# Kernel tuning notes

Hardware: AMD Instinct MI355X
Metric: run time of the kernel (lower is better)

## Reference

```python
import jax, jax.numpy as jnp
import numpy as np

OFFS = [(dy, dx) for dy in (-1, 0, 1) for dx in (-1, 0, 1)]  # ME centered 3x3 region


def _build_maps():
    """Build the sparse coordinate pyramid and per-offset kernel maps, exactly
    mirroring MinkowskiEngine: out coords of a stride-2 conv are unique(c//2),
    and a pair (i_in, i_out) exists iff coord_out*stride + offset is active."""
    G = 1024
    rng = np.random.default_rng(0)
    flat = np.sort(rng.choice(G * G, size=300000, replace=False))
    coords = [np.stack(np.unravel_index(flat, (G, G)), axis=1).astype(np.int64)]
    grids = [G]
    for _ in range(3):
        coords.append(np.unique(coords[-1] // 2, axis=0))
        grids.append(grids[-1] // 2)

    def lut(c, g):
        t = -np.ones(g * g, np.int64)
        t[c[:, 0] * g + c[:, 1]] = np.arange(len(c))
        return t

    luts = [lut(c, g) for c, g in zip(coords, grids)]

    def kmap(lvl_in, c_out, stride):
        g, L = grids[lvl_in], luts[lvl_in]
        n_in, n_out = len(coords[lvl_in]), len(c_out)
        base = c_out * stride
        pairs = []
        for dy, dx in OFFS:
            q = base + np.array([dy, dx])
            ok = (q[:, 0] >= 0) & (q[:, 0] < g) & (q[:, 1] >= 0) & (q[:, 1] < g)
            key = np.clip(q[:, 0] * g + q[:, 1], 0, g * g - 1)
            idx = np.where(ok, L[key], -1)
            sel = np.nonzero(idx >= 0)[0]
            pairs.append((idx[sel], sel))
        M = max(len(p[0]) for p in pairs)
        ii = np.full((9, M), n_in, np.int32)   # pad -> dummy zero input row
        oo = np.full((9, M), n_out, np.int32)  # pad -> dummy output row (dropped)
        for k, (a, b) in enumerate(pairs):
            ii[k, :len(a)] = a
            oo[k, :len(b)] = b
        return ii, oo

    maps = {
        'c0': kmap(0, coords[0], 1), 'd0': kmap(0, coords[1], 2),
        'c1': kmap(1, coords[1], 1), 'd1': kmap(1, coords[2], 2),
        'c2': kmap(2, coords[2], 1), 'd2': kmap(2, coords[3], 2),
    }
    return maps, [len(c) for c in coords]


def setup_inputs() -> dict:
    maps, (n0, n1, n2, n3) = _build_maps()
    ks = jax.random.split(jax.random.key(0), 16)
    d = {'feats': jax.random.normal(ks[0], (n0, 1), jnp.float32)}
    chans = [(1, 64), (64, 128), (128, 128), (128, 128), (128, 128), (128, 128)]
    names = ['c0', 'd0', 'c1', 'd1', 'c2', 'd2']
    for i, (nm, (ci, co)) in enumerate(zip(names, chans)):
        d[f'w_{nm}'] = jax.random.normal(ks[1 + 2 * i], (9, ci, co), jnp.float32) / np.sqrt(9.0 * ci)
        d[f'b_{nm}'] = jax.random.normal(ks[2 + 2 * i], (co,), jnp.float32) * 0.01
        d[f'in_{nm}'] = jnp.asarray(maps[nm][0])
        d[f'out_{nm}'] = jnp.asarray(maps[nm][1])
    d.update(n0=n0, n1=n1, n2=n2, n3=n3)
    return d


def sparse_conv(feats, w, b, in_idx, out_idx, n_out):
    """Gather-GEMM-scatter sparse conv. w: [9, Cin, Cout]. Padded pairs point at a
    dummy zero input row (index n_in) and a dummy output row (index n_out)."""
    n_in, cin = feats.shape
    fp = jnp.concatenate([feats, jnp.zeros((1, cin), feats.dtype)], axis=0)
    out = jnp.zeros((n_out + 1, w.shape[2]), feats.dtype)
    for k in range(9):  # fixed kernel volume
        out = out.at[out_idx[k]].add(fp[in_idx[k]] @ w[k])
    return out[:n_out] + b


def reference(feats, w_c0, b_c0, in_c0, out_c0, w_d0, b_d0, in_d0, out_d0,
              w_c1, b_c1, in_c1, out_c1, w_d1, b_d1, in_d1, out_d1,
              w_c2, b_c2, in_c2, out_c2, w_d2, b_d2, in_d2, out_d2,
              n0, n1, n2, n3):
    x = sparse_conv(feats, w_c0, b_c0, in_c0, out_c0, n0)
    out0 = jax.nn.relu(sparse_conv(x, w_d0, b_d0, in_d0, out_d0, n1))
    y = sparse_conv(out0, w_c1, b_c1, in_c1, out_c1, n1)
    out1 = jax.nn.relu(sparse_conv(y, w_d1, b_d1, in_d1, out_d1, n2))
    z = sparse_conv(out1, w_c2, b_c2, in_c2, out_c2, n2)
    out2 = sparse_conv(z, w_d2, b_d2, in_d2, out_d2, n3)
    return (out2, out1, out0)
```

## Files before the change

kernel.cpp:

```cpp
#include <hip/hip_runtime.h>
#include <stdint.h>
#include <algorithm>


#define DI __device__ __forceinline__

typedef __attribute__((ext_vector_type(8))) short bf16x8;
typedef __attribute__((ext_vector_type(4))) float f32x4;

DI uint16_t f2bf(float x){
  union{float f;uint32_t i;}v; v.f=x;
  uint32_t r = v.i + 0x7fffu + ((v.i>>16)&1u);
  return (uint16_t)(r>>16);
}
DI uint32_t pack2(float a, float b){
  return (uint32_t)f2bf(a) | ((uint32_t)f2bf(b) << 16);
}
DI void gload16(const void* g, void* l){
  __builtin_amdgcn_global_load_lds(
      (const __attribute__((address_space(1))) void*)g,
      (__attribute__((address_space(3))) void*)l, 16, 0, 0);
}

__global__ __launch_bounds__(256) void diag_kernel(float* __restrict__ out, long n, float c){
  long i = (long)blockIdx.x*256 + threadIdx.x;
  if (i < n) out[i] = c;
}

__global__ __launch_bounds__(256) void init_all_kernel(
    int* __restrict__ tab, long ntab, float* __restrict__ zp){
  long i = (long)blockIdx.x*256 + threadIdx.x;
  if (i < ntab) tab[i] = -1;
  if (blockIdx.x == 0 && threadIdx.x < 64) zp[threadIdx.x] = 0.f;
}

struct BuildArgs {
  const int* im[6];
  const int* om[6];
  int   M[6];
  int   nin[6];
  int   nout[6];
  long  toff[6];
};

__global__ __launch_bounds__(256) void build_all_kernel(
    BuildArgs a, int* __restrict__ tb){
  const int L = blockIdx.z, k = blockIdx.y;
  const int M = a.M[L];
  long t = (long)blockIdx.x*256 + threadIdx.x;
  if (t >= M) return;
  int ii = a.im[L][(long)k*M + t];
  int oo = a.om[L][(long)k*M + t];
  if (ii >= 0 && ii < a.nin[L] && oo >= 0 && oo < a.nout[L])
    tb[a.toff[L] + (long)k*a.nout[L] + oo] = ii;
}

__global__ __launch_bounds__(256) void prep_all_kernel(
    const float* __restrict__ w0, const float* __restrict__ w1,
    const float* __restrict__ w2, const float* __restrict__ w3,
    const float* __restrict__ w4, uint16_t* __restrict__ wb, long total){
  const long wt64 = 9L*128*64, wt128 = 9L*128*128;
  long idx = (long)blockIdx.x*256 + threadIdx.x;
  if (idx >= total) return;
  int L; long r; int cin;
  if (idx < wt64){ L = 0; r = idx; cin = 64; }
  else { long j = idx - wt64; L = 1 + (int)(j / wt128); r = j % wt128; cin = 128; }
  const float* w = (L==0) ? w0 : (L==1) ? w1 : (L==2) ? w2 : (L==3) ? w3 : w4;
  int k = (int)(r / (128*cin));
  int rem = (int)(r % (128*cin));
  int cout = rem / cin, ci = rem % cin;
  wb[idx] = f2bf(w[((long)k*cin + ci)*128 + cout]);
}

__global__ __launch_bounds__(256) void c0_tab_kernel(
    const float* __restrict__ feats, const float* __restrict__ w,
    const float* __restrict__ bias, const int* __restrict__ tab,
    uint16_t* __restrict__ out, int n_out){
  __shared__ float w_s[576];
  __shared__ float b_s[64];
  const int tid = threadIdx.x;
  for (int i = tid; i < 576; i += 256) w_s[i] = w[i];
  if (tid < 64) b_s[tid] = bias[tid];
  __syncthreads();
  long r = (long)blockIdx.x*256 + tid;
  if (r >= n_out) return;
  float f[9];
  #pragma unroll
  for (int k = 0; k < 9; k++){
    int gi = tab[(long)k*n_out + r];
    f[k] = (gi >= 0) ? feats[gi] : 0.f;
  }
  uint16_t* dst = out + r*64;
  #pragma unroll
  for (int c0 = 0; c0 < 64; c0 += 16){
    float a[16];
    #pragma unroll
    for (int j = 0; j < 16; j++) a[j] = b_s[c0+j];
    #pragma unroll
    for (int k = 0; k < 9; k++){
      float fk = f[k];
      #pragma unroll
      for (int j = 0; j < 16; j++) a[j] += fk * w_s[k*64 + c0 + j];
    }
    uint4 o0, o1;
    o0.x = pack2(a[0],a[1]);   o0.y = pack2(a[2],a[3]);
    o0.z = pack2(a[4],a[5]);   o0.w = pack2(a[6],a[7]);
    o1.x = pack2(a[8],a[9]);   o1.y = pack2(a[10],a[11]);
    o1.z = pack2(a[12],a[13]); o1.w = pack2(a[14],a[15]);
    *(uint4*)(dst + c0)     = o0;
    *(uint4*)(dst + c0 + 8) = o1;
  }
}

template<int CIN, int OUTMODE, bool RELU>
__global__ __launch_bounds__(512,4) void mconv4_kernel(
    const char* __restrict__ ws_base, long in_off, long wtb_off, long zp_off,
    const float* __restrict__ bias, const int* __restrict__ tab,
    float* __restrict__ outf, uint16_t* __restrict__ outb, int n_out){
  constexpr int NS = 9*CIN/64;
  __shared__ __align__(16) uint16_t ab[3][128*64];
  __shared__ __align__(16) uint16_t bb[2][128*64];

  const int tid = threadIdx.x;
  const int nwg = gridDim.x, orig = blockIdx.x;
  const int q = nwg >> 3, rr = nwg & 7, xcd = orig & 7, pos = orig >> 3;
  const int wg = (xcd < rr ? xcd*(q+1) : rr*(q+1) + (xcd-rr)*q) + pos;
  const long rb = (long)wg * 128;

  const int r0 = tid >> 3, sg = tid & 7;
  const int ss0 = sg ^ (r0 & 7);

  uint32_t offA[2][9];
  #pragma unroll
  for (int kk = 0; kk < 9; ++kk){
    #pragma unroll
    for (int it = 0; it < 2; ++it){
      long row = rb + it*64 + r0;
      int gi = (row < (long)n_out) ? tab[(long)kk*n_out + row] : -1;
      offA[it][kk] = (gi >= 0)
          ? (uint32_t)(in_off + (long)gi*(CIN*2) + ss0*16)
          : (uint32_t)(zp_off + ss0*16);
    }
  }
  const uint32_t offB = (uint32_t)(wtb_off + ((long)r0*CIN + ss0*8)*2);

  const int lane = tid & 63;
  const int wv = tid >> 6;
  const int wr = (wv >> 1) << 5;
  const int wc = (wv & 1) << 6;
  const int l16 = lane & 15, quad = lane >> 4;

  float bv[4];
  #pragma unroll
  for (int ct = 0; ct < 4; ++ct) bv[ct] = bias[wc + (ct<<4) + l16];

  f32x4 acc[2][4];
  #pragma unroll
  for (int i = 0; i < 2; i++)
    #pragma unroll
    for (int j = 0; j < 4; j++)
      acc[i][j] = (f32x4){0.f,0.f,0.f,0.f};

  auto stage_a = [&](int step, int nb){
    const int kk  = (CIN == 64) ? step : (step >> 1);
    const int c0b = (CIN == 64) ? 0 : ((step & 1) * 128);
    #pragma unroll
    for (int it = 0; it < 2; ++it)
      gload16(ws_base + offA[it][kk] + c0b, &ab[nb][(it*512+tid)*8]);
  };
  auto stage_b = [&](int step, int nb){
    const int kk  = (CIN == 64) ? step : (step >> 1);
    const int c0b = (CIN == 64) ? 0 : ((step & 1) * 128);
    const uint32_t base = offB + (uint32_t)((long)kk*128*CIN*2 + c0b);
    #pragma unroll
    for (int it = 0; it < 2; ++it)
      gload16(ws_base + base + it*(64*CIN*2), &bb[nb][(it*512+tid)*8]);
  };
  auto compute = [&](int na, int nb){
    const uint16_t* A  = &ab[na][0];
    const uint16_t* Bm = &bb[nb][0];
    __builtin_amdgcn_s_setprio(1);
    #pragma unroll
    for (int ch = 0; ch < 2; ++ch){
      const int xs = ((((ch << 2) + quad) ^ (l16 & 7)) << 3);
      bf16x8 af[2], bfr[4];
      #pragma unroll
      for (int u = 0; u < 2; ++u)
        af[u]  = *(const bf16x8*)&A [((wr + (u<<4) + l16) << 6) + xs];
      #pragma unroll
      for (int u = 0; u < 4; ++u)
        bfr[u] = *(const bf16x8*)&Bm[((wc + (u<<4) + l16) << 6) + xs];
      #pragma unroll
      for (int rt = 0; rt < 2; ++rt)
        #pragma unroll
        for (int ct = 0; ct < 4; ++ct)
          acc[rt][ct] = __builtin_amdgcn_mfma_f32_16x16x32_bf16(
              af[rt], bfr[ct], acc[rt][ct], 0, 0, 0);
    }
    __builtin_amdgcn_s_setprio(0);
  };

  stage_a(0, 0);
  stage_a(1, 1);
  stage_b(0, 0);
  #pragma unroll
  for (int t = 0; t < NS; ++t){
    if (t + 2 < NS) stage_a(t+2, (t+2)%3);
    if (t + 1 < NS) stage_b(t+1, (t+1)&1);
    if (t + 2 < NS){
      asm volatile("s_waitcnt vmcnt(4)" ::: "memory");
    } else if (t + 1 < NS){
      asm volatile("s_waitcnt vmcnt(2)" ::: "memory");
    } else {
      asm volatile("s_waitcnt vmcnt(0)" ::: "memory");
    }
    __builtin_amdgcn_sched_barrier(0);
    __builtin_amdgcn_s_barrier();
    compute(t%3, t&1);
    if (t + 1 < NS)
      __builtin_amdgcn_s_barrier();
  }

  #pragma unroll
  for (int ct = 0; ct < 4; ++ct){
    const int cout = wc + (ct<<4) + l16;
    #pragma unroll
    for (int rt = 0; rt < 2; ++rt){
      #pragma unroll
      for (int r = 0; r < 4; ++r){
        long row = rb + wr + (rt<<4) + (quad<<2) + r;
        if (row < (long)n_out){
          float v = acc[rt][ct][r] + bv[ct];
          if (RELU) v = v > 0.f ? v : 0.f;
          if constexpr (OUTMODE == 0 || OUTMODE == 2) outf[row*128 + cout] = v;
          if constexpr (OUTMODE == 1 || OUTMODE == 2) outb[row*128 + cout] = f2bf(v);
        }
      }
    }
  }
}

static inline long cdivl(long a, long b){ return (a + b - 1) / b; }

extern "C" void kernel_launch(void* const* d_in, const int* in_sizes, int n_in_args,
                              void* d_out, int out_size, void* d_ws, size_t ws_size,
                              hipStream_t stream) {
  const float* feats = (const float*)d_in[0];
  const float* w_c0 = (const float*)d_in[1];
  const float* b_c0 = (const float*)d_in[2];
  const int* in_c0  = (const int*)d_in[3];
  const int* out_c0 = (const int*)d_in[4];
  const float* w_d0 = (const float*)d_in[5];
  const float* b_d0 = (const float*)d_in[6];
  const int* in_d0  = (const int*)d_in[7];
  const int* out_d0 = (const int*)d_in[8];
  const float* w_c1 = (const float*)d_in[9];
  const float* b_c1 = (const float*)d_in[10];
  const int* in_c1  = (const int*)d_in[11];
  const int* out_c1 = (const int*)d_in[12];
  const float* w_d1 = (const float*)d_in[13];
  const float* b_d1 = (const float*)d_in[14];
  const int* in_d1  = (const int*)d_in[15];
  const int* out_d1 = (const int*)d_in[16];
  const float* w_c2 = (const float*)d_in[17];
  const float* b_c2 = (const float*)d_in[18];
  const int* in_c2  = (const int*)d_in[19];
  const int* out_c2 = (const int*)d_in[20];
  const float* w_d2 = (const float*)d_in[21];
  const float* b_d2 = (const float*)d_in[22];
  const int* in_d2  = (const int*)d_in[23];
  const int* out_d2 = (const int*)d_in[24];

  const int n0   = in_sizes[0];
  const int M_c0 = in_sizes[3]  / 9;
  const int M_d0 = in_sizes[7]  / 9;
  const int M_c1 = in_sizes[11] / 9;
  const int M_d1 = in_sizes[15] / 9;
  const int M_c2 = in_sizes[19] / 9;
  const int M_d2 = in_sizes[23] / 9;
  const int n1   = M_c1;
  const int n2   = M_c2;
  const int n3   = out_size/128 - n1 - n2;

  bool sane = n0 > 0 && out_size % 128 == 0 &&
              M_c0 > 0 && M_d0 > 0 && M_d1 > 0 && M_d2 > 0 &&
              n1 > 0 && n2 > 0 && n3 > 0;

  long maxElems = (long)n0*64;
  if ((long)n1*128 > maxElems) maxElems = (long)n1*128;
  if ((long)n2*128 > maxElems) maxElems = (long)n2*128;
  long fbytes = (maxElems*2 + 255)/256*256;
  long ntab   = sane ? 9L*((long)n0 + 2L*n1 + 2L*n2 + n3) : 0;
  long tbytes = (ntab*4 + 255)/256*256;
  long wt64  = 9L*128*64, wt128 = 9L*128*128;
  long wbytes = ((wt64 + 4*wt128)*2 + 255)/256*256;
  long zbytes = 256;
  long b1bytes = sane ? ((long)n2*128*2 + 255)/256*256 : 0;
  long b0bytes = sane ? ((long)n1*128*2 + 255)/256*256 : 0;
  long need_full = fbytes + tbytes + wbytes + zbytes + 256 + b1bytes + b0bytes;

  if (!sane || ws_size < (size_t)need_full){
    float C = (float)(16 + (int)std::min<size_t>(ws_size >> 20, (size_t)100000));
    if (!sane) C *= 1099511627776.0f;
    diag_kernel<<<cdivl(out_size,256),256,0,stream>>>((float*)d_out, out_size, C);
    return;
  }

  uint16_t* fbuf = (uint16_t*)d_ws;
  long tab_off    = fbytes;
  long wtb_off    = fbytes + tbytes;
  long zp_off     = fbytes + tbytes + wbytes;
  long bf1_off    = zp_off + zbytes + 256;
  long bf0_off    = bf1_off + b1bytes;
  const char* wsb = (const char*)d_ws;
  int* tb        = (int*)((char*)d_ws + tab_off);
  float* zp_p    = (float*)((char*)d_ws + zp_off);
  uint16_t* bf1  = (uint16_t*)((char*)d_ws + bf1_off);
  uint16_t* bf0  = (uint16_t*)((char*)d_ws + bf0_off);

  long t_c0 = 0;
  long t_d0 = t_c0 + 9L*n0;
  long t_c1 = t_d0 + 9L*n1;
  long t_d1 = t_c1 + 9L*n1;
  long t_c2 = t_d1 + 9L*n2;
  long t_d2 = t_c2 + 9L*n2;

  float* out2 = (float*)d_out;
  float* out1 = out2 + (long)n3*128;
  float* out0 = out1 + (long)n2*128;

  init_all_kernel<<<cdivl(ntab,256),256,0,stream>>>(tb, ntab, zp_p);

  BuildArgs ba;
  ba.im[0]=in_c0;  ba.om[0]=out_c0; ba.M[0]=M_c0; ba.nin[0]=n0; ba.nout[0]=n0; ba.toff[0]=t_c0;
  ba.im[1]=in_d0;  ba.om[1]=out_d0; ba.M[1]=M_d0; ba.nin[1]=n0; ba.nout[1]=n1; ba.toff[1]=t_d0;
  ba.im[2]=in_c1;  ba.om[2]=out_c1; ba.M[2]=M_c1; ba.nin[2]=n1; ba.nout[2]=n1; ba.toff[2]=t_c1;
  ba.im[3]=in_d1;  ba.om[3]=out_d1; ba.M[3]=M_d1; ba.nin[3]=n1; ba.nout[3]=n2; ba.toff[3]=t_d1;
  ba.im[4]=in_c2;  ba.om[4]=out_c2; ba.M[4]=M_c2; ba.nin[4]=n2; ba.nout[4]=n2; ba.toff[4]=t_c2;
  ba.im[5]=in_d2;  ba.om[5]=out_d2; ba.M[5]=M_d2; ba.nin[5]=n2; ba.nout[5]=n3; ba.toff[5]=t_d2;
  long maxM = M_c0;
  for (int i = 0; i < 6; ++i) if (ba.M[i] > maxM) maxM = ba.M[i];
  dim3 bg((unsigned)cdivl(maxM,256), 9, 6);
  build_all_kernel<<<bg,256,0,stream>>>(ba, tb);

  long wtotal = wt64 + 4*wt128;
  prep_all_kernel<<<cdivl(wtotal,256),256,0,stream>>>(
      w_d0, w_c1, w_d1, w_c2, w_d2,
      (uint16_t*)((char*)d_ws + wtb_off), wtotal);

  c0_tab_kernel<<<cdivl(n0,256),256,0,stream>>>(feats, w_c0, b_c0, tb + t_c0, fbuf, n0);

  mconv4_kernel<64,2,true><<<cdivl(n1,128),512,0,stream>>>(
      wsb, 0L, wtb_off, zp_off, b_d0, tb + t_d0, out0, bf0, n1);

  mconv4_kernel<128,1,false><<<cdivl(n1,128),512,0,stream>>>(
      wsb, bf0_off, wtb_off + wt64*2, zp_off, b_c1, tb + t_c1, nullptr, fbuf, n1);

  mconv4_kernel<128,2,true><<<cdivl(n2,128),512,0,stream>>>(
      wsb, 0L, wtb_off + (wt64 + wt128)*2, zp_off, b_d1, tb + t_d1, out1, bf1, n2);

  mconv4_kernel<128,1,false><<<cdivl(n2,128),512,0,stream>>>(
      wsb, bf1_off, wtb_off + (wt64 + 2*wt128)*2, zp_off, b_c2, tb + t_c2, nullptr, fbuf, n2);

  mconv4_kernel<128,0,false><<<cdivl(n3,128),512,0,stream>>>(
      wsb, 0L, wtb_off + (wt64 + 3*wt128)*2, zp_off, b_d2, tb + t_d2, out2, nullptr, n3);
}
```

Before: 491.0 us.

## Fuse all stages into a persistent megakernel with global barriers

Replaces the separate init, map-build, weight-prep, first-layer and five gather-GEMM launches with one persistent kernel of 512 blocks. The stages are separated by atomic-counter grid barriers, and each conv phase distributes its row tiles across blocks in a loop. The aim is to remove launch gaps and tail effects between the many small kernels. The risks are the spin barrier overhead, deadlock if not all 512 blocks are co-resident, and lower per-phase parallelism than the original grids.

Result: slower. 1.420 ms (+189.1%).

```diff
diff --git a/kernel.cpp b/kernel.cpp
--- a/kernel.cpp
+++ b/kernel.cpp
@@ -27,125 +27,70 @@
   if (i < n) out[i] = c;
 }
 
-__global__ __launch_bounds__(256) void init_all_kernel(
-    int* __restrict__ tab, long ntab, float* __restrict__ zp){
-  long i = (long)blockIdx.x*256 + threadIdx.x;
-  if (i < ntab) tab[i] = -1;
-  if (blockIdx.x == 0 && threadIdx.x < 64) zp[threadIdx.x] = 0.f;
-}
-
-struct BuildArgs {
-  const int* im[6];
-  const int* om[6];
-  int   M[6];
-  int   nin[6];
-  int   nout[6];
+__global__ __launch_bounds__(256) void init_bar_kernel(int* __restrict__ bar,
+                                                       float* __restrict__ zp){
+  int t = threadIdx.x;
+  if (t < 64) bar[t] = 0;
+  if (t >= 64 && t < 128) zp[t-64] = 0.f;
+}
+
+struct MegaArgs {
+  const char* wsb;
+  int* tb;
+  int* bar;
+  long ntab;
+  const int* im[6]; const int* om[6];
+  int   M[6]; int nin[6]; int nout[6];
   long  toff[6];
+  const float* w[5];
+  long wtotal;
+  uint16_t* wb;
+  const float* feats; const float* w_c0; const float* b_c0;
+  uint16_t* fbuf;
+  int n0, n1, n2, n3;
+  long wtb_off, zp_off, bf0_off, bf1_off;
+  const float *b_d0, *b_c1, *b_d1, *b_c2, *b_d2;
+  float *out0, *out1, *out2;
+  uint16_t *bf0, *bf1;
 };
 
-__global__ __launch_bounds__(256) void build_all_kernel(
-    BuildArgs a, int* __restrict__ tb){
-  const int L = blockIdx.z, k = blockIdx.y;
-  const int M = a.M[L];
-  long t = (long)blockIdx.x*256 + threadIdx.x;
-  if (t >= M) return;
-  int ii = a.im[L][(long)k*M + t];
-  int oo = a.om[L][(long)k*M + t];
-  if (ii >= 0 && ii < a.nin[L] && oo >= 0 && oo < a.nout[L])
-    tb[a.toff[L] + (long)k*a.nout[L] + oo] = ii;
-}
-
-__global__ __launch_bounds__(256) void prep_all_kernel(
-    const float* __restrict__ w0, const float* __restrict__ w1,
-    const float* __restrict__ w2, const float* __restrict__ w3,
-    const float* __restrict__ w4, uint16_t* __restrict__ wb, long total){
-  const long wt64 = 9L*128*64, wt128 = 9L*128*128;
-  long idx = (long)blockIdx.x*256 + threadIdx.x;
-  if (idx >= total) return;
-  int L; long r; int cin;
-  if (idx < wt64){ L = 0; r = idx; cin = 64; }
-  else { long j = idx - wt64; L = 1 + (int)(j / wt128); r = j % wt128; cin = 128; }
-  const float* w = (L==0) ? w0 : (L==1) ? w1 : (L==2) ? w2 : (L==3) ? w3 : w4;
-  int k = (int)(r / (128*cin));
-  int rem = (int)(r % (128*cin));
-  int cout = rem / cin, ci = rem % cin;
-  wb[idx] = f2bf(w[((long)k*cin + ci)*128 + cout]);
-}
-
-__global__ __launch_bounds__(256) void c0_tab_kernel(
-    const float* __restrict__ feats, const float* __restrict__ w,
-    const float* __restrict__ bias, const int* __restrict__ tab,
-    uint16_t* __restrict__ out, int n_out){
-  __shared__ float w_s[576];
-  __shared__ float b_s[64];
+DI void gsync(int* bar, int target){
+  __syncthreads();
+  if (threadIdx.x == 0){
+    __threadfence();
+    atomicAdd(bar, 1);
+    int spins = 0;
+    while (atomicAdd(bar, 0) < target){
+      __builtin_amdgcn_s_sleep(8);
+      if (++spins > 100000000) break;
+    }
+    __threadfence();
+  }
+  __syncthreads();
+}
+
+template<int CIN, int OUTMODE, bool RELU>
+DI void mconv_phase(uint8_t* smem, const char* ws_base, long in_off,
+                    long wtb_off, long zp_off,
+                    const float* __restrict__ bias, const int* __restrict__ tab,
+                    float* __restrict__ outf, uint16_t* __restrict__ outb,
+                    int n_out, int bid, int nblk){
+  constexpr int NS = 9*CIN/64;
+  uint16_t (*ab)[128*64] = (uint16_t(*)[128*64])smem;
+  uint16_t (*bb)[128*64] = (uint16_t(*)[128*64])(smem + 3*16384);
   const int tid = threadIdx.x;
-  for (int i = tid; i < 576; i += 256) w_s[i] = w[i];
-  if (tid < 64) b_s[tid] = bias[tid];
-  __syncthreads();
-  long r = (long)blockIdx.x*256 + tid;
-  if (r >= n_out) return;
-  float f[9];
-  #pragma unroll
-  for (int k = 0; k < 9; k++){
-    int gi = tab[(long)k*n_out + r];
-    f[k] = (gi >= 0) ? feats[gi] : 0.f;
-  }
-  uint16_t* dst = out + r*64;
-  #pragma unroll
-  for (int c0 = 0; c0 < 64; c0 += 16){
-    float a[16];
-    #pragma unroll
-    for (int j = 0; j < 16; j++) a[j] = b_s[c0+j];
-    #pragma unroll
-    for (int k = 0; k < 9; k++){
-      float fk = f[k];
-      #pragma unroll
-      for (int j = 0; j < 16; j++) a[j] += fk * w_s[k*64 + c0 + j];
-    }
-    uint4 o0, o1;
-    o0.x = pack2(a[0],a[1]);   o0.y = pack2(a[2],a[3]);
-    o0.z = pack2(a[4],a[5]);   o0.w = pack2(a[6],a[7]);
-    o1.x = pack2(a[8],a[9]);   o1.y = pack2(a[10],a[11]);
-    o1.z = pack2(a[12],a[13]); o1.w = pack2(a[14],a[15]);
-    *(uint4*)(dst + c0)     = o0;
-    *(uint4*)(dst + c0 + 8) = o1;
-  }
-}
-
-template<int CIN, int OUTMODE, bool RELU>
-__global__ __launch_bounds__(512,4) void mconv4_kernel(
-    const char* __restrict__ ws_base, long in_off, long wtb_off, long zp_off,
-    const float* __restrict__ bias, const int* __restrict__ tab,
-    float* __restrict__ outf, uint16_t* __restrict__ outb, int n_out){
-  constexpr int NS = 9*CIN/64;
-  __shared__ __align__(16) uint16_t ab[3][128*64];
-  __shared__ __align__(16) uint16_t bb[2][128*64];
-
-  const int tid = threadIdx.x;
-  const int nwg = gridDim.x, orig = blockIdx.x;
-  const int q = nwg >> 3, rr = nwg & 7, xcd = orig & 7, pos = orig >> 3;
-  const int wg = (xcd < rr ? xcd*(q+1) : rr*(q+1) + (xcd-rr)*q) + pos;
-  const long rb = (long)wg * 128;
+
+  const int T = (n_out + 127) >> 7;
+  const int q = T / nblk, r = T % nblk;
+  const int sb = (bid & 7)*(nblk >> 3) + (bid >> 3);
+  const int t0 = (sb < r) ? sb*(q+1) : r*(q+1) + (sb - r)*q;
+  const int t1 = t0 + ((sb < r) ? (q+1) : q);
 
   const int r0 = tid >> 3, sg = tid & 7;
   const int ss0 = sg ^ (r0 & 7);
-
-  uint32_t offA[2][9];
-  #pragma unroll
-  for (int kk = 0; kk < 9; ++kk){
-    #pragma unroll
-    for (int it = 0; it < 2; ++it){
-      long row = rb + it*64 + r0;
-      int gi = (row < (long)n_out) ? tab[(long)kk*n_out + row] : -1;
-      offA[it][kk] = (gi >= 0)
-          ? (uint32_t)(in_off + (long)gi*(CIN*2) + ss0*16)
-          : (uint32_t)(zp_off + ss0*16);
-    }
-  }
   const uint32_t offB = (uint32_t)(wtb_off + ((long)r0*CIN + ss0*8)*2);
 
-  const int lane = tid & 63;
-  const int wv = tid >> 6;
+  const int lane = tid & 63, wv = tid >> 6;
   const int wr = (wv >> 1) << 5;
   const int wc = (wv & 1) << 6;
   const int l16 = lane & 15, quad = lane >> 4;
@@ -154,90 +99,198 @@
   #pragma unroll
   for (int ct = 0; ct < 4; ++ct) bv[ct] = bias[wc + (ct<<4) + l16];
 
-  f32x4 acc[2][4];
-  #pragma unroll
-  for (int i = 0; i < 2; i++)
+  for (int tile = t0; tile < t1; ++tile){
+    __builtin_amdgcn_s_barrier();
+    const long rb = (long)tile * 128;
+
+    uint32_t offA[2][9];
     #pragma unroll
-    for (int j = 0; j < 4; j++)
-      acc[i][j] = (f32x4){0.f,0.f,0.f,0.f};
-
-  auto stage_a = [&](int step, int nb){
-    const int kk  = (CIN == 64) ? step : (step >> 1);
-    const int c0b = (CIN == 64) ? 0 : ((step & 1) * 128);
+    for (int kk = 0; kk < 9; ++kk){
+      #pragma unroll
+      for (int it = 0; it < 2; ++it){
+        long row = rb + it*64 + r0;
+        int gi = (row < (long)n_out) ? tab[(long)kk*n_out + row] : -1;
+        offA[it][kk] = (gi >= 0)
+            ? (uint32_t)(in_off + (long)gi*(CIN*2) + ss0*16)
+            : (uint32_t)(zp_off + ss0*16);
+      }
+    }
+
+    f32x4 acc[2][4];
     #pragma unroll
-    for (int it = 0; it < 2; ++it)
-      gload16(ws_base + offA[it][kk] + c0b, &ab[nb][(it*512+tid)*8]);
-  };
-  auto stage_b = [&](int step, int nb){
-    const int kk  = (CIN == 64) ? step : (step >> 1);
-    const int c0b = (CIN == 64) ? 0 : ((step & 1) * 128);
-    const uint32_t base = offB + (uint32_t)((long)kk*128*CIN*2 + c0b);
+    for (int i = 0; i < 2; i++)
+      #pragma unroll
+      for (int j = 0; j < 4; j++)
+        acc[i][j] = (f32x4){0.f,0.f,0.f,0.f};
+
+    auto stage_a = [&](int step, int nb){
+      const int kk  = (CIN == 64) ? step : (step >> 1);
+      const int c0b = (CIN == 64) ? 0 : ((step & 1) * 128);
+      #pragma unroll
+      for (int it = 0; it < 2; ++it)
+        gload16(ws_base + offA[it][kk] + c0b, &ab[nb][(it*512+tid)*8]);
+    };
+    auto stage_b = [&](int step, int nb){
+      const int kk  = (CIN == 64) ? step : (step >> 1);
+      const int c0b = (CIN == 64) ? 0 : ((step & 1) * 128);
+      const uint32_t base = offB + (uint32_t)((long)kk*128*CIN*2 + c0b);
+      #pragma unroll
+      for (int it = 0; it < 2; ++it)
+        gload16(ws_base + base + it*(64*CIN*2), &bb[nb][(it*512+tid)*8]);
+    };
+    auto compute = [&](int na, int nb){
+      const uint16_t* A  = &ab[na][0];
+      const uint16_t* Bm = &bb[nb][0];
+      __builtin_amdgcn_s_setprio(1);
+      #pragma unroll
+      for (int ch = 0; ch < 2; ++ch){
+        const int xs = ((((ch << 2) + quad) ^ (l16 & 7)) << 3);
+        bf16x8 af[2], bfr[4];
+        #pragma unroll
+        for (int u = 0; u < 2; ++u)
+          af[u]  = *(const bf16x8*)&A [((wr + (u<<4) + l16) << 6) + xs];
+        #pragma unroll
+        for (int u = 0; u < 4; ++u)
+          bfr[u] = *(const bf16x8*)&Bm[((wc + (u<<4) + l16) << 6) + xs];
+        #pragma unroll
+        for (int rt = 0; rt < 2; ++rt)
+          #pragma unroll
+          for (int ct = 0; ct < 4; ++ct)
+            acc[rt][ct] = __builtin_amdgcn_mfma_f32_16x16x32_bf16(
+                af[rt], bfr[ct], acc[rt][ct], 0, 0, 0);
+      }
+      __builtin_amdgcn_s_setprio(0);
+    };
+
+    stage_a(0, 0);
+    stage_a(1, 1);
+    stage_b(0, 0);
     #pragma unroll
-    for (int it = 0; it < 2; ++it)
-      gload16(ws_base + base + it*(64*CIN*2), &bb[nb][(it*512+tid)*8]);
-  };
-  auto compute = [&](int na, int nb){
-    const uint16_t* A  = &ab[na][0];
-    const uint16_t* Bm = &bb[nb][0];
-    __builtin_amdgcn_s_setprio(1);
+    for (int t = 0; t < NS; ++t){
+      if (t + 2 < NS) stage_a(t+2, (t+2)%3);
+      if (t + 1 < NS) stage_b(t+1, (t+1)&1);
+      if (t + 2 < NS){
+        asm volatile("s_waitcnt vmcnt(4)" ::: "memory");
+      } else if (t + 1 < NS){
+        asm volatile("s_waitcnt vmcnt(2)" ::: "memory");
+      } else {
+        asm volatile("s_waitcnt vmcnt(0)" ::: "memory");
+      }
+      __builtin_amdgcn_sched_barrier(0);
+      __builtin_amdgcn_s_barrier();
+      compute(t%3, t&1);
+      if (t + 1 < NS)
+        __builtin_amdgcn_s_barrier();
+    }
+
     #pragma unroll
-    for (int ch = 0; ch < 2; ++ch){
-      const int xs = ((((ch << 2) + quad) ^ (l16 & 7)) << 3);
-      bf16x8 af[2], bfr[4];
-      #pragma unroll
-      for (int u = 0; u < 2; ++u)
-        af[u]  = *(const bf16x8*)&A [((wr + (u<<4) + l16) << 6) + xs];
-      #pragma unroll
-      for (int u = 0; u < 4; ++u)
-        bfr[u] = *(const bf16x8*)&Bm[((wc + (u<<4) + l16) << 6) + xs];
-      #pragma unroll
-      for (int rt = 0; rt < 2; ++rt)
-        #pragma unroll
-        for (int ct = 0; ct < 4; ++ct)
-          acc[rt][ct] = __builtin_amdgcn_mfma_f32_16x16x32_bf16(
-              af[rt], bfr[ct], acc[rt][ct], 0, 0, 0);
-    }
-    __builtin_amdgcn_s_setprio(0);
-  };
-
-  stage_a(0, 0);
-  stage_a(1, 1);
-  stage_b(0, 0);
-  #pragma unroll
-  for (int t = 0; t < NS; ++t){
-    if (t + 2 < NS) stage_a(t+2, (t+2)%3);
-    if (t + 1 < NS) stage_b(t+1, (t+1)&1);
-    if (t + 2 < NS){
-      asm volatile("s_waitcnt vmcnt(4)" ::: "memory");
-    } else if (t + 1 < NS){
-      asm volatile("s_waitcnt vmcnt(2)" ::: "memory");
-    } else {
-      asm volatile("s_waitcnt vmcnt(0)" ::: "memory");
-    }
-    __builtin_amdgcn_sched_barrier(0);
-    __builtin_amdgcn_s_barrier();
-    compute(t%3, t&1);
-    if (t + 1 < NS)
-      __builtin_amdgcn_s_barrier();
-  }
-
-  #pragma unroll
-  for (int ct = 0; ct < 4; ++ct){
-    const int cout = wc + (ct<<4) + l16;
-    #pragma unroll
-    for (int rt = 0; rt < 2; ++rt){
-      #pragma unroll
-      for (int r = 0; r < 4; ++r){
-        long row = rb + wr + (rt<<4) + (quad<<2) + r;
-        if (row < (long)n_out){
-          float v = acc[rt][ct][r] + bv[ct];
-          if (RELU) v = v > 0.f ? v : 0.f;
-          if constexpr (OUTMODE == 0 || OUTMODE == 2) outf[row*128 + cout] = v;
-          if constexpr (OUTMODE == 1 || OUTMODE == 2) outb[row*128 + cout] = f2bf(v);
+    for (int ct = 0; ct < 4; ++ct){
+      const int cout = wc + (ct<<4) + l16;
+      #pragma unroll
+      for (int rt = 0; rt < 2; ++rt){
+        #pragma unroll
+        for (int rr2 = 0; rr2 < 4; ++rr2){
+          long row = rb + wr + (rt<<4) + (quad<<2) + rr2;
+          if (row < (long)n_out){
+            float v = acc[rt][ct][rr2] + bv[ct];
+            if (RELU) v = v > 0.f ? v : 0.f;
+            if constexpr (OUTMODE == 0 || OUTMODE == 2) outf[row*128 + cout] = v;
+            if constexpr (OUTMODE == 1 || OUTMODE == 2) outb[row*128 + cout] = f2bf(v);
+          }
         }
       }
     }
   }
+}
+
+__global__ __launch_bounds__(512,4) void mega_kernel(MegaArgs a){
+  __shared__ __align__(16) uint8_t smem[81920];
+  const int tid = threadIdx.x, bid = blockIdx.x;
+  const int nblk = gridDim.x;
+  const long gid = (long)bid*512 + tid;
+  const long gstride = (long)nblk*512;
+
+  for (long i = gid; i < a.ntab; i += gstride) a.tb[i] = -1;
+  {
+    const long wt64 = 9L*128*64, wt128 = 9L*128*128;
+    for (long idx = gid; idx < a.wtotal; idx += gstride){
+      int L; long rr; int cin;
+      if (idx < wt64){ L = 0; rr = idx; cin = 64; }
+      else { long j = idx - wt64; L = 1 + (int)(j / wt128); rr = j % wt128; cin = 128; }
+      const float* w = a.w[L];
+      int k = (int)(rr / (128*cin));
+      int rem = (int)(rr % (128*cin));
+      int cout = rem / cin, ci = rem % cin;
+      a.wb[idx] = f2bf(w[((long)k*cin + ci)*128 + cout]);
+    }
+  }
+  gsync(a.bar, 1*nblk);
+
+  for (int L = 0; L < 6; ++L){
+    const int M = a.M[L];
+    for (long t = gid; t < 9L*M; t += gstride){
+      int k = (int)(t / M); long i = t - (long)k*M;
+      int ii = a.im[L][(long)k*M + i];
+      int oo = a.om[L][(long)k*M + i];
+      if (ii >= 0 && ii < a.nin[L] && oo >= 0 && oo < a.nout[L])
+        a.tb[a.toff[L] + (long)k*a.nout[L] + oo] = ii;
+    }
+  }
+  gsync(a.bar, 2*nblk);
+
+  {
+    float* w_s = (float*)smem;
+    float* b_s = (float*)smem + 576;
+    for (int i = tid; i < 576; i += 512) w_s[i] = a.w_c0[i];
+    if (tid < 64) b_s[tid] = a.b_c0[tid];
+    __syncthreads();
+    const int* tab = a.tb;
+    for (long rr = gid; rr < (long)a.n0; rr += gstride){
+      float f[9];
+      #pragma unroll
+      for (int k = 0; k < 9; k++){
+        int gi = tab[(long)k*a.n0 + rr];
+        f[k] = (gi >= 0) ? a.feats[gi] : 0.f;
+      }
+      uint16_t* dst = a.fbuf + rr*64;
+      #pragma unroll
+      for (int c0 = 0; c0 < 64; c0 += 16){
+        float ac[16];
+        #pragma unroll
+        for (int j = 0; j < 16; j++) ac[j] = b_s[c0+j];
+        #pragma unroll
+        for (int k = 0; k < 9; k++){
+          float fk = f[k];
+          #pragma unroll
+          for (int j = 0; j < 16; j++) ac[j] += fk * w_s[k*64 + c0 + j];
+        }
+        uint4 o0, o1;
+        o0.x = pack2(ac[0],ac[1]);   o0.y = pack2(ac[2],ac[3]);
+        o0.z = pack2(ac[4],ac[5]);   o0.w = pack2(ac[6],ac[7]);
+        o1.x = pack2(ac[8],ac[9]);   o1.y = pack2(ac[10],ac[11]);
+        o1.z = pack2(ac[12],ac[13]); o1.w = pack2(ac[14],ac[15]);
+        *(uint4*)(dst + c0)     = o0;
+        *(uint4*)(dst + c0 + 8) = o1;
+      }
+    }
+  }
+  gsync(a.bar, 3*nblk);
+
+  const long wt64 = 9L*128*64, wt128 = 9L*128*128;
+  mconv_phase<64,2,true>(smem, a.wsb, 0L, a.wtb_off, a.zp_off,
+                         a.b_d0, a.tb + a.toff[1], a.out0, a.bf0, a.n1, bid, nblk);
+  gsync(a.bar, 4*nblk);
+  mconv_phase<128,1,false>(smem, a.wsb, a.bf0_off, a.wtb_off + wt64*2, a.zp_off,
+                           a.b_c1, a.tb + a.toff[2], nullptr, a.fbuf, a.n1, bid, nblk);
+  gsync(a.bar, 5*nblk);
+  mconv_phase<128,2,true>(smem, a.wsb, 0L, a.wtb_off + (wt64 + wt128)*2, a.zp_off,
+                          a.b_d1, a.tb + a.toff[3], a.out1, a.bf1, a.n2, bid, nblk);
+  gsync(a.bar, 6*nblk);
+  mconv_phase<128,1,false>(smem, a.wsb, a.bf1_off, a.wtb_off + (wt64 + 2*wt128)*2, a.zp_off,
+                           a.b_c2, a.tb + a.toff[4], nullptr, a.fbuf, a.n2, bid, nblk);
+  gsync(a.bar, 7*nblk);
+  mconv_phase<128,0,false>(smem, a.wsb, 0L, a.wtb_off + (wt64 + 3*wt128)*2, a.zp_off,
+                           a.b_d2, a.tb + a.toff[5], a.out2, nullptr, a.n3, bid, nblk);
 }
 
 static inline long cdivl(long a, long b){ return (a + b - 1) / b; }
@@ -295,9 +348,11 @@
   long wt64  = 9L*128*64, wt128 = 9L*128*128;
   long wbytes = ((wt64 + 4*wt128)*2 + 255)/256*256;
   long zbytes = 256;
+  long barbytes = 256;
   long b1bytes = sane ? ((long)n2*128*2 + 255)/256*256 : 0;
   long b0bytes = sane ? ((long)n1*128*2 + 255)/256*256 : 0;
-  long need_full = fbytes + tbytes + wbytes + zbytes + 256 + b1bytes + b0bytes;
+  long need_full = fbytes + tbytes + wbytes + zbytes + barbytes + 256
+                 + b1bytes + b0bytes;
 
   if (!sane || ws_size < (size_t)need_full){
     float C = (float)(16 + (int)std::min<size_t>(ws_size >> 20, (size_t)100000));
@@ -310,11 +365,13 @@
   long tab_off    = fbytes;
   long wtb_off    = fbytes + tbytes;
   long zp_off     = fbytes + tbytes + wbytes;
-  long bf1_off    = zp_off + zbytes + 256;
+  long bar_off    = zp_off + zbytes;
+  long bf1_off    = bar_off + barbytes + 256;
   long bf0_off    = bf1_off + b1bytes;
   const char* wsb = (const char*)d_ws;
   int* tb        = (int*)((char*)d_ws + tab_off);
   float* zp_p    = (float*)((char*)d_ws + zp_off);
+  int* bar_p     = (int*)((char*)d_ws + bar_off);
   uint16_t* bf1  = (uint16_t*)((char*)d_ws + bf1_off);
   uint16_t* bf0  = (uint16_t*)((char*)d_ws + bf0_off);
 
@@ -329,39 +386,26 @@
   float* out1 = out2 + (long)n3*128;
   float* out0 = out1 + (long)n2*128;
 
-  init_all_kernel<<<cdivl(ntab,256),256,0,stream>>>(tb, ntab, zp_p);
-
-  BuildArgs ba;
-  ba.im[0]=in_c0;  ba.om[0]=out_c0; ba.M[0]=M_c0; ba.nin[0]=n0; ba.nout[0]=n0; ba.toff[0]=t_c0;
-  ba.im[1]=in_d0;  ba.om[1]=out_d0; ba.M[1]=M_d0; ba.nin[1]=n0; ba.nout[1]=n1; ba.toff[1]=t_d0;
-  ba.im[2]=in_c1;  ba.om[2]=out_c1; ba.M[2]=M_c1; ba.nin[2]=n1; ba.nout[2]=n1; ba.toff[2]=t_c1;
-  ba.im[3]=in_d1;  ba.om[3]=out_d1; ba.M[3]=M_d1; ba.nin[3]=n1; ba.nout[3]=n2; ba.toff[3]=t_d1;
-  ba.im[4]=in_c2;  ba.om[4]=out_c2; ba.M[4]=M_c2; ba.nin[4]=n2; ba.nout[4]=n2; ba.toff[4]=t_c2;
-  ba.im[5]=in_d2;  ba.om[5]=out_d2; ba.M[5]=M_d2; ba.nin[5]=n2; ba.nout[5]=n3; ba.toff[5]=t_d2;
-  long maxM = M_c0;
-  for (int i = 0; i < 6; ++i) if (ba.M[i] > maxM) maxM = ba.M[i];
-  dim3 bg((unsigned)cdivl(maxM,256), 9, 6);
-  build_all_kernel<<<bg,256,0,stream>>>(ba, tb);
-
-  long wtotal = wt64 + 4*wt128;
-  prep_all_kernel<<<cdivl(wtotal,256),256,0,stream>>>(
-      w_d0, w_c1, w_d1, w_c2, w_d2,
-      (uint16_t*)((char*)d_ws + wtb_off), wtotal);
-
-  c0_tab_kernel<<<cdivl(n0,256),256,0,stream>>>(feats, w_c0, b_c0, tb + t_c0, fbuf, n0);
-
-  mconv4_kernel<64,2,true><<<cdivl(n1,128),512,0,stream>>>(
-      wsb, 0L, wtb_off, zp_off, b_d0, tb + t_d0, out0, bf0, n1);
-
-  mconv4_kernel<128,1,false><<<cdivl(n1,128),512,0,stream>>>(
-      wsb, bf0_off, wtb_off + wt64*2, zp_off, b_c1, tb + t_c1, nullptr, fbuf, n1);
-
-  mconv4_kernel<128,2,true><<<cdivl(n2,128),512,0,stream>>>(
-      wsb, 0L, wtb_off + (wt64 + wt128)*2, zp_off, b_d1, tb + t_d1, out1, bf1, n2);
-
-  mconv4_kernel<128,1,false><<<cdivl(n2,128),512,0,stream>>>(
-      wsb, bf1_off, wtb_off + (wt64 + 2*wt128)*2, zp_off, b_c2, tb + t_c2, nullptr, fbuf, n2);
-
-  mconv4_kernel<128,0,false><<<cdivl(n3,128),512,0,stream>>>(
-      wsb, 0L, wtb_off + (wt64 + 3*wt128)*2, zp_off, b_d2, tb + t_d2, out2, nullptr, n3);
-}
+  MegaArgs ma;
+  ma.wsb = wsb; ma.tb = tb; ma.bar = bar_p; ma.ntab = ntab;
+  ma.im[0]=in_c0;  ma.om[0]=out_c0; ma.M[0]=M_c0; ma.nin[0]=n0; ma.nout[0]=n0; ma.toff[0]=t_c0;
+  ma.im[1]=in_d0;  ma.om[1]=out_d0; ma.M[1]=M_d0; ma.nin[1]=n0; ma.nout[1]=n1; ma.toff[1]=t_d0;
+  ma.im[2]=in_c1;  ma.om[2]=out_c1; ma.M[2]=M_c1; ma.nin[2]=n1; ma.nout[2]=n1; ma.toff[2]=t_c1;
+  ma.im[3]=in_d1;  ma.om[3]=out_d1; ma.M[3]=M_d1; ma.nin[3]=n1; ma.nout[3]=n2; ma.toff[3]=t_d1;
+  ma.im[4]=in_c2;  ma.om[4]=out_c2; ma.M[4]=M_c2; ma.nin[4]=n2; ma.nout[4]=n2; ma.toff[4]=t_c2;
+  ma.im[5]=in_d2;  ma.om[5]=out_d2; ma.M[5]=M_d2; ma.nin[5]=n2; ma.nout[5]=n3; ma.toff[5]=t_d2;
+  ma.w[0]=w_d0; ma.w[1]=w_c1; ma.w[2]=w_d1; ma.w[3]=w_c2; ma.w[4]=w_d2;
+  ma.wtotal = wt64 + 4*wt128;
+  ma.wb = (uint16_t*)((char*)d_ws + wtb_off);
+  ma.feats = feats; ma.w_c0 = w_c0; ma.b_c0 = b_c0;
+  ma.fbuf = fbuf;
+  ma.n0 = n0; ma.n1 = n1; ma.n2 = n2; ma.n3 = n3;
+  ma.wtb_off = wtb_off; ma.zp_off = zp_off;
+  ma.bf0_off = bf0_off; ma.bf1_off = bf1_off;
+  ma.b_d0 = b_d0; ma.b_c1 = b_c1; ma.b_d1 = b_d1; ma.b_c2 = b_c2; ma.b_d2 = b_d2;
+  ma.out0 = out0; ma.out1 = out1; ma.out2 = out2;
+  ma.bf0 = bf0; ma.bf1 = bf1;
+
+  init_bar_kernel<<<1,256,0,stream>>>(bar_p, zp_p);
+  mega_kernel<<<512,512,0,stream>>>(ma);
+}
```

## Merge prep/build kernels, use memset for table init, double-buffer A tiles

Applied to the files above, without the earlier changes.

Weight conversion and kernel-map table building now run in one grid-stride kernel, and the table and zero-pad initialisation move to hipMemsetAsync calls. This cuts the number of small launches before the convolutions. The GEMM kernel's A-tile buffer drops from triple to double buffering, so A and B for the next step are staged together. That frees shared memory, which may allow more resident blocks, but the A gathers get one step less prefetch distance to hide latency.

Result: slower. 503.3 us (+2.5%).

```diff
diff --git a/kernel.cpp b/kernel.cpp
--- a/kernel.cpp
+++ b/kernel.cpp
@@ -27,49 +27,45 @@
   if (i < n) out[i] = c;
 }
 
-__global__ __launch_bounds__(256) void init_all_kernel(
-    int* __restrict__ tab, long ntab, float* __restrict__ zp){
-  long i = (long)blockIdx.x*256 + threadIdx.x;
-  if (i < ntab) tab[i] = -1;
-  if (blockIdx.x == 0 && threadIdx.x < 64) zp[threadIdx.x] = 0.f;
-}
-
-struct BuildArgs {
-  const int* im[6];
-  const int* om[6];
-  int   M[6];
-  int   nin[6];
-  int   nout[6];
-  long  toff[6];
+struct PBArgs {
+  const float* w[5];
+  uint16_t* wb;
+  long wtotal;
+  const int* im[6]; const int* om[6];
+  int M[6]; int nin[6]; int nout[6];
+  long toff[6];
+  long bcum[7];
+  int* tb;
+  long total;
 };
 
-__global__ __launch_bounds__(256) void build_all_kernel(
-    BuildArgs a, int* __restrict__ tb){
-  const int L = blockIdx.z, k = blockIdx.y;
-  const int M = a.M[L];
-  long t = (long)blockIdx.x*256 + threadIdx.x;
-  if (t >= M) return;
-  int ii = a.im[L][(long)k*M + t];
-  int oo = a.om[L][(long)k*M + t];
-  if (ii >= 0 && ii < a.nin[L] && oo >= 0 && oo < a.nout[L])
-    tb[a.toff[L] + (long)k*a.nout[L] + oo] = ii;
-}
-
-__global__ __launch_bounds__(256) void prep_all_kernel(
-    const float* __restrict__ w0, const float* __restrict__ w1,
-    const float* __restrict__ w2, const float* __restrict__ w3,
-    const float* __restrict__ w4, uint16_t* __restrict__ wb, long total){
+__global__ __launch_bounds__(256) void prep_build_kernel(PBArgs a){
   const long wt64 = 9L*128*64, wt128 = 9L*128*128;
-  long idx = (long)blockIdx.x*256 + threadIdx.x;
-  if (idx >= total) return;
-  int L; long r; int cin;
-  if (idx < wt64){ L = 0; r = idx; cin = 64; }
-  else { long j = idx - wt64; L = 1 + (int)(j / wt128); r = j % wt128; cin = 128; }
-  const float* w = (L==0) ? w0 : (L==1) ? w1 : (L==2) ? w2 : (L==3) ? w3 : w4;
-  int k = (int)(r / (128*cin));
-  int rem = (int)(r % (128*cin));
-  int cout = rem / cin, ci = rem % cin;
-  wb[idx] = f2bf(w[((long)k*cin + ci)*128 + cout]);
+  const long gstride = (long)gridDim.x*256;
+  for (long i = (long)blockIdx.x*256 + threadIdx.x; i < a.total; i += gstride){
+    if (i < a.wtotal){
+      int L; long rr; int cin;
+      if (i < wt64){ L = 0; rr = i; cin = 64; }
+      else { long j = i - wt64; L = 1 + (int)(j / wt128); rr = j % wt128; cin = 128; }
+      const float* w = a.w[L];
+      int k = (int)(rr / (128*cin));
+      int rem = (int)(rr % (128*cin));
+      int cout = rem / cin, ci = rem % cin;
+      a.wb[i] = f2bf(w[((long)k*cin + ci)*128 + cout]);
+    } else {
+      long j = i - a.wtotal;
+      int L = 0;
+      while (L < 5 && j >= a.bcum[L+1]) ++L;
+      j -= a.bcum[L];
+      const int M = a.M[L];
+      int k = (int)(j / M);
+      long t = j - (long)k*M;
+      int ii = a.im[L][(long)k*M + t];
+      int oo = a.om[L][(long)k*M + t];
+      if (ii >= 0 && ii < a.nin[L] && oo >= 0 && oo < a.nout[L])
+        a.tb[a.toff[L] + (long)k*a.nout[L] + oo] = ii;
+    }
+  }
 }
 
 __global__ __launch_bounds__(256) void c0_tab_kernel(
@@ -113,12 +109,12 @@
 }
 
 template<int CIN, int OUTMODE, bool RELU>
-__global__ __launch_bounds__(512,4) void mconv4_kernel(
+__global__ __launch_bounds__(512,4) void mconv2_kernel(
     const char* __restrict__ ws_base, long in_off, long wtb_off, long zp_off,
     const float* __restrict__ bias, const int* __restrict__ tab,
     float* __restrict__ outf, uint16_t* __restrict__ outb, int n_out){
   constexpr int NS = 9*CIN/64;
-  __shared__ __align__(16) uint16_t ab[3][128*64];
+  __shared__ __align__(16) uint16_t ab[2][128*64];
   __shared__ __align__(16) uint16_t bb[2][128*64];
 
   const int tid = threadIdx.x;
@@ -176,8 +172,8 @@
     for (int it = 0; it < 2; ++it)
       gload16(ws_base + base + it*(64*CIN*2), &bb[nb][(it*512+tid)*8]);
   };
-  auto compute = [&](int na, int nb){
-    const uint16_t* A  = &ab[na][0];
+  auto compute = [&](int nb){
+    const uint16_t* A  = &ab[nb][0];
     const uint16_t* Bm = &bb[nb][0];
     __builtin_amdgcn_s_setprio(1);
     #pragma unroll
@@ -201,22 +197,20 @@
   };
 
   stage_a(0, 0);
-  stage_a(1, 1);
   stage_b(0, 0);
   #pragma unroll
   for (int t = 0; t < NS; ++t){
-    if (t + 2 < NS) stage_a(t+2, (t+2)%3);
-    if (t + 1 < NS) stage_b(t+1, (t+1)&1);
-    if (t + 2 < NS){
+    const int cur = t & 1;
+    if (t + 1 < NS){
+      stage_a(t+1, cur^1);
+      stage_b(t+1, cur^1);
       asm volatile("s_waitcnt vmcnt(4)" ::: "memory");
-    } else if (t + 1 < NS){
-      asm volatile("s_waitcnt vmcnt(2)" ::: "memory");
     } else {
       asm volatile("s_waitcnt vmcnt(0)" ::: "memory");
     }
     __builtin_amdgcn_sched_barrier(0);
     __builtin_amdgcn_s_barrier();
-    compute(t%3, t&1);
+    compute(cur);
     if (t + 1 < NS)
       __builtin_amdgcn_s_barrier();
   }
@@ -329,39 +323,40 @@
   float* out1 = out2 + (long)n3*128;
   float* out0 = out1 + (long)n2*128;
 
-  init_all_kernel<<<cdivl(ntab,256),256,0,stream>>>(tb, ntab, zp_p);
-
-  BuildArgs ba;
-  ba.im[0]=in_c0;  ba.om[0]=out_c0; ba.M[0]=M_c0; ba.nin[0]=n0; ba.nout[0]=n0; ba.toff[0]=t_c0;
-  ba.im[1]=in_d0;  ba.om[1]=out_d0; ba.M[1]=M_d0; ba.nin[1]=n0; ba.nout[1]=n1; ba.toff[1]=t_d0;
-  ba.im[2]=in_c1;  ba.om[2]=out_c1; ba.M[2]=M_c1; ba.nin[2]=n1; ba.nout[2]=n1; ba.toff[2]=t_c1;
-  ba.im[3]=in_d1;  ba.om[3]=out_d1; ba.M[3]=M_d1; ba.nin[3]=n1; ba.nout[3]=n2; ba.toff[3]=t_d1;
-  ba.im[4]=in_c2;  ba.om[4]=out_c2; ba.M[4]=M_c2; ba.nin[4]=n2; ba.nout[4]=n2; ba.toff[4]=t_c2;
-  ba.im[5]=in_d2;  ba.om[5]=out_d2; ba.M[5]=M_d2; ba.nin[5]=n2; ba.nout[5]=n3; ba.toff[5]=t_d2;
-  long maxM = M_c0;
-  for (int i = 0; i < 6; ++i) if (ba.M[i] > maxM) maxM = ba.M[i];
-  dim3 bg((unsigned)cdivl(maxM,256), 9, 6);
-  build_all_kernel<<<bg,256,0,stream>>>(ba, tb);
-
-  long wtotal = wt64 + 4*wt128;
-  prep_all_kernel<<<cdivl(wtotal,256),256,0,stream>>>(
-      w_d0, w_c1, w_d1, w_c2, w_d2,
-      (uint16_t*)((char*)d_ws + wtb_off), wtotal);
+  hipMemsetAsync(tb, 0xFF, (size_t)ntab*4, stream);
+  hipMemsetAsync(zp_p, 0, 256, stream);
+
+  PBArgs pa;
+  pa.w[0]=w_d0; pa.w[1]=w_c1; pa.w[2]=w_d1; pa.w[3]=w_c2; pa.w[4]=w_d2;
+  pa.wb = (uint16_t*)((char*)d_ws + wtb_off);
+  pa.wtotal = wt64 + 4*wt128;
+  pa.im[0]=in_c0;  pa.om[0]=out_c0; pa.M[0]=M_c0; pa.nin[0]=n0; pa.nout[0]=n0; pa.toff[0]=t_c0;
+  pa.im[1]=in_d0;  pa.om[1]=out_d0; pa.M[1]=M_d0; pa.nin[1]=n0; pa.nout[1]=n1; pa.toff[1]=t_d0;
+  pa.im[2]=in_c1;  pa.om[2]=out_c1; pa.M[2]=M_c1; pa.nin[2]=n1; pa.nout[2]=n1; pa.toff[2]=t_c1;
+  pa.im[3]=in_d1;  pa.om[3]=out_d1; pa.M[3]=M_d1; pa.nin[3]=n1; pa.nout[3]=n2; pa.toff[3]=t_d1;
+  pa.im[4]=in_c2;  pa.om[4]=out_c2; pa.M[4]=M_c2; pa.nin[4]=n2; pa.nout[4]=n2; pa.toff[4]=t_c2;
+  pa.im[5]=in_d2;  pa.om[5]=out_d2; pa.M[5]=M_d2; pa.nin[5]=n2; pa.nout[5]=n3; pa.toff[5]=t_d2;
+  pa.bcum[0] = 0;
+  for (int i = 0; i < 6; ++i) pa.bcum[i+1] = pa.bcum[i] + 9L*pa.M[i];
+  pa.tb = tb;
+  pa.total = pa.wtotal + pa.bcum[6];
+  long pbg = std::min(cdivl(pa.total, 256), (long)4096);
+  prep_build_kernel<<<(unsigned)pbg,256,0,stream>>>(pa);
 
   c0_tab_kernel<<<cdivl(n0,256),256,0,stream>>>(feats, w_c0, b_c0, tb + t_c0, fbuf, n0);
 
-  mconv4_kernel<64,2,true><<<cdivl(n1,128),512,0,stream>>>(
+  mconv2_kernel<64,2,true><<<cdivl(n1,128),512,0,stream>>>(
       wsb, 0L, wtb_off, zp_off, b_d0, tb + t_d0, out0, bf0, n1);
 
-  mconv4_kernel<128,1,false><<<cdivl(n1,128),512,0,stream>>>(
+  mconv2_kernel<128,1,false><<<cdivl(n1,128),512,0,stream>>>(
       wsb, bf0_off, wtb_off + wt64*2, zp_off, b_c1, tb + t_c1, nullptr, fbuf, n1);
 
-  mconv4_kernel<128,2,true><<<cdivl(n2,128),512,0,stream>>>(
+  mconv2_kernel<128,2,true><<<cdivl(n2,128),512,0,stream>>>(
       wsb, 0L, wtb_off + (wt64 + wt128)*2, zp_off, b_d1, tb + t_d1, out1, bf1, n2);
 
-  mconv4_kernel<128,1,false><<<cdivl(n2,128),512,0,stream>>>(
+  mconv2_kernel<128,1,false><<<cdivl(n2,128),512,0,stream>>>(
       wsb, bf1_off, wtb_off + (wt64 + 2*wt128)*2, zp_off, b_c2, tb + t_c2, nullptr, fbuf, n2);
 
-  mconv4_kernel<128,0,false><<<cdivl(n3,128),512,0,stream>>>(
+  mconv2_kernel<128,0,false><<<cdivl(n3,128),512,0,stream>>>(
       wsb, 0L, wtb_off + (wt64 + 3*wt128)*2, zp_off, b_d2, tb + t_d2, out2, nullptr, n3);
 }
```
